# Optimization experiments

Measured on AMD Instinct MI355X. Metric: run time of the kernel, lower is better.

Reference implementation:

```python
import jax, jax.numpy as jnp
import numpy as np

SPS = 16
SPAN = 8
BETA = 0.5


def design_rrc(sps, span, beta):
    """Root-raised-cosine FIR taps, unit energy, shape (K,) float32."""
    num_taps = sps * span
    t = np.arange(num_taps) - (num_taps - 1) / 2
    ts = t / sps
    with np.errstate(divide='ignore', invalid='ignore'):
        num = np.sin(np.pi * ts * (1 - beta)) + 4 * beta * ts * np.cos(np.pi * ts * (1 + beta))
        den = np.pi * ts * (1 - (4 * beta * ts) ** 2)
        rrc = num / den
    rrc[np.isnan(rrc)] = 1.0
    energy = np.sum(rrc ** 2)
    if energy > 1e-15:
        rrc = rrc / np.sqrt(energy)
    return jnp.asarray(rrc, dtype=jnp.float32)


def setup_inputs() -> dict:
    key = jax.random.key(0)
    bits = jax.random.randint(key, (256, 16384), 0, 2, dtype=jnp.int32)
    rrc = design_rrc(SPS, SPAN, BETA)  # (128,)
    return {"bits": bits, "rrc": rrc}


def reference(bits, rrc):
    sps = SPS
    B, num_bits = bits.shape
    ns = num_bits // 2
    b2 = bits.reshape(B, ns, 2)
    # Gray map: (0,0)->(+1+1j), (0,1)->(-1+1j), (1,1)->(-1-1j), (1,0)->(+1-1j), /sqrt(2)
    inv_sqrt2 = jnp.float32(1.0 / np.sqrt(2.0))
    re = (1 - 2 * b2[..., 1]).astype(jnp.float32) * inv_sqrt2  # (B, ns)
    im = (1 - 2 * b2[..., 0]).astype(jnp.float32) * inv_sqrt2  # (B, ns)
    sym = jnp.stack([re, im], axis=1)  # (B, 2, ns) channels = [real, imag]

    up_len = ns * sps
    offset = sps // 2
    # zero-stuff upsample with half-sps right shift (pad-left-then-truncate in original)
    up = jnp.zeros((B, 2, up_len), jnp.float32).at[:, :, offset::sps].set(sym)

    K = rrc.shape[0]
    pad_l = (K - 1) // 2
    pad_r = K - 1 - pad_l
    kern = jnp.broadcast_to(rrc[None, None, :], (2, 1, K))  # depthwise, same taps for I/Q
    y = jax.lax.conv_general_dilated(
        up, kern, window_strides=(1,), padding=[(pad_l, pad_r)],
        feature_group_count=2)  # (B, 2, up_len), cross-correlation like torch conv1d
    y = y * jnp.float32(np.sqrt(sps))
    return jnp.transpose(y, (0, 2, 1))  # (B, up_len, 2) = [real, imag]
```

## Files before the change

### kernel.cpp

```cpp
#include <hip/hip_runtime.h>

#define SPS    16
#define NS     8192
#define NBITS  16384
#define UPLEN  (NS * SPS)
#define KTAPS  128
#define QPB    256

__global__ __launch_bounds__(256)
void qpsk_mod_kernel(const int* __restrict__ bits,
                     const float* __restrict__ rrc,
                     float* __restrict__ out) {
    __shared__ float s_taps[KTAPS];
    __shared__ float s_re[QPB + 9];
    __shared__ float s_im[QPB + 9];

    const int tid = threadIdx.x;
    const int b   = blockIdx.x >> 5;
    const int q0  = (blockIdx.x & 31) * QPB;

    if (tid < KTAPS) s_taps[tid] = rrc[tid];

    const float scale = 2.82842712474619f;
    for (int ls = tid; ls < QPB + 9; ls += 256) {
        int s = q0 - 4 + ls;
        float re = 0.f, im = 0.f;
        if (s >= 0 && s < NS) {
            int b0 = bits[b * NBITS + 2 * s];
            int b1 = bits[b * NBITS + 2 * s + 1];
            re = (float)(1 - 2 * b1) * scale;
            im = (float)(1 - 2 * b0) * scale;
        }
        s_re[ls] = re;
        s_im[ls] = im;
    }
    __syncthreads();

    const int loc = tid;
    float acc_re[16], acc_im[16];
#pragma unroll
    for (int p = 0; p < 16; ++p) { acc_re[p] = 0.f; acc_im[p] = 0.f; }

#pragma unroll
    for (int i = 0; i < 8; ++i) {
        float tt[16];
#pragma unroll
        for (int j = 0; j < 4; ++j) {
            float4 v = *(const float4*)(&s_taps[16 * i + 4 * j]);
            tt[4 * j + 0] = v.x; tt[4 * j + 1] = v.y;
            tt[4 * j + 2] = v.z; tt[4 * j + 3] = v.w;
        }
        float sa_re = s_re[loc + i];
        float sa_im = s_im[loc + i];
        float sb_re = s_re[loc + i + 1];
        float sb_im = s_im[loc + i + 1];
#pragma unroll
        for (int p = 0; p < 8; ++p) {
            float t = tt[7 - p];
            acc_re[p] += t * sa_re;
            acc_im[p] += t * sa_im;
        }
#pragma unroll
        for (int p = 8; p < 16; ++p) {
            float t = tt[23 - p];
            acc_re[p] += t * sb_re;
            acc_im[p] += t * sb_im;
        }
    }

    float* outp = out + (size_t)b * (UPLEN * 2) + (size_t)(q0 + loc) * 32;
#pragma unroll
    for (int p = 0; p < 16; p += 2) {
        float4 v = make_float4(acc_re[p], acc_im[p], acc_re[p + 1], acc_im[p + 1]);
        *(float4*)(outp + 2 * p) = v;
    }
}

extern "C" void kernel_launch(void* const* d_in, const int* in_sizes, int n_in,
                              void* d_out, int out_size, void* d_ws, size_t ws_size,
                              hipStream_t stream) {
    const int*   bits = (const int*)d_in[0];
    const float* rrc  = (const float*)d_in[1];
    float*       out  = (float*)d_out;

    const int B = in_sizes[0] / NBITS;
    dim3 grid(B * (NS / QPB));
    qpsk_mod_kernel<<<grid, 256, 0, stream>>>(bits, rrc, out);
}
```

Before: 321.9 us.

## Remap threads so each writes float4 at consecutive addresses for coalesced stores

Each thread now produces one output phase pair for eight consecutive symbols, instead of one symbol's 16 phases. The mapping is arranged so that adjacent lanes write adjacent float4s, which coalesces global stores. Taps are loaded into registers once, the symbol window is read with vector LDS loads, and bit pairs are read as int2. In exchange there are more per-thread select operations and a different register footprint.

```diff
diff --git a/kernel.cpp b/kernel.cpp
--- a/kernel.cpp
+++ b/kernel.cpp
@@ -6,14 +6,15 @@
 #define UPLEN  (NS * SPS)
 #define KTAPS  128
 #define QPB    256
+#define SWIN   264
 
 __global__ __launch_bounds__(256)
 void qpsk_mod_kernel(const int* __restrict__ bits,
                      const float* __restrict__ rrc,
                      float* __restrict__ out) {
     __shared__ float s_taps[KTAPS];
-    __shared__ float s_re[QPB + 9];
-    __shared__ float s_im[QPB + 9];
+    __shared__ float s_re[SWIN];
+    __shared__ float s_im[SWIN];
 
     const int tid = threadIdx.x;
     const int b   = blockIdx.x >> 5;
@@ -22,57 +23,62 @@
     if (tid < KTAPS) s_taps[tid] = rrc[tid];
 
     const float scale = 2.82842712474619f;
-    for (int ls = tid; ls < QPB + 9; ls += 256) {
+    for (int ls = tid; ls < SWIN; ls += 256) {
         int s = q0 - 4 + ls;
         float re = 0.f, im = 0.f;
         if (s >= 0 && s < NS) {
-            int b0 = bits[b * NBITS + 2 * s];
-            int b1 = bits[b * NBITS + 2 * s + 1];
-            re = (float)(1 - 2 * b1) * scale;
-            im = (float)(1 - 2 * b0) * scale;
+            int2 bb = *(const int2*)(bits + b * NBITS + 2 * s);
+            re = (float)(1 - 2 * bb.y) * scale;
+            im = (float)(1 - 2 * bb.x) * scale;
         }
         s_re[ls] = re;
         s_im[ls] = im;
     }
     __syncthreads();
 
-    const int loc = tid;
-    float acc_re[16], acc_im[16];
-#pragma unroll
-    for (int p = 0; p < 16; ++p) { acc_re[p] = 0.f; acc_im[p] = 0.f; }
+    const int k = tid & 7;
+    const int g = tid >> 3;
+    const int off = (k < 4) ? (6 - 2 * k) : (22 - 2 * k);
+    const bool hi_half = (k >= 4);
 
+    float tlo[8], thi[8];
 #pragma unroll
     for (int i = 0; i < 8; ++i) {
-        float tt[16];
-#pragma unroll
-        for (int j = 0; j < 4; ++j) {
-            float4 v = *(const float4*)(&s_taps[16 * i + 4 * j]);
-            tt[4 * j + 0] = v.x; tt[4 * j + 1] = v.y;
-            tt[4 * j + 2] = v.z; tt[4 * j + 3] = v.w;
-        }
-        float sa_re = s_re[loc + i];
-        float sa_im = s_im[loc + i];
-        float sb_re = s_re[loc + i + 1];
-        float sb_im = s_im[loc + i + 1];
-#pragma unroll
-        for (int p = 0; p < 8; ++p) {
-            float t = tt[7 - p];
-            acc_re[p] += t * sa_re;
-            acc_im[p] += t * sa_im;
-        }
-#pragma unroll
-        for (int p = 8; p < 16; ++p) {
-            float t = tt[23 - p];
-            acc_re[p] += t * sb_re;
-            acc_im[p] += t * sb_im;
-        }
+        float2 tp = *(const float2*)(&s_taps[16 * i + off]);
+        tlo[i] = tp.x;
+        thi[i] = tp.y;
     }
 
-    float* outp = out + (size_t)b * (UPLEN * 2) + (size_t)(q0 + loc) * 32;
+    float wre[16], wim[16];
 #pragma unroll
-    for (int p = 0; p < 16; p += 2) {
-        float4 v = make_float4(acc_re[p], acc_im[p], acc_re[p + 1], acc_im[p + 1]);
-        *(float4*)(outp + 2 * p) = v;
+    for (int j = 0; j < 16; j += 4) {
+        float4 vr = *(const float4*)(&s_re[g * 8 + j]);
+        wre[j] = vr.x; wre[j + 1] = vr.y; wre[j + 2] = vr.z; wre[j + 3] = vr.w;
+        float4 vi = *(const float4*)(&s_im[g * 8 + j]);
+        wim[j] = vi.x; wim[j + 1] = vi.y; wim[j + 2] = vi.z; wim[j + 3] = vi.w;
+    }
+    float sre[15], sim[15];
+#pragma unroll
+    for (int j = 0; j < 15; ++j) {
+        sre[j] = hi_half ? wre[j + 1] : wre[j];
+        sim[j] = hi_half ? wim[j + 1] : wim[j];
+    }
+
+    float* outp = out + (size_t)b * (UPLEN * 2)
+                      + (size_t)(q0 + g * 8) * 32 + 4 * k;
+#pragma unroll
+    for (int r = 0; r < 8; ++r) {
+        float a0 = 0.f, a1 = 0.f, a2 = 0.f, a3 = 0.f;
+#pragma unroll
+        for (int i = 0; i < 8; ++i) {
+            float sr = sre[r + i];
+            float si = sim[r + i];
+            a0 += thi[i] * sr;
+            a1 += thi[i] * si;
+            a2 += tlo[i] * sr;
+            a3 += tlo[i] * si;
+        }
+        *(float4*)(outp + 32 * r) = make_float4(a0, a1, a2, a3);
     }
 }
 
```

Result: no change. 316.7 us (-1.6%).
